# Kernel tuning notes

Hardware: AMD Instinct MI355X
Metric: run time of the kernel (lower is better)

## Reference

```python
import jax, jax.numpy as jnp
import numpy as np

RADIUS = 0.2
NPOINT = 1024
NSAMPLE = 32


def _square_distance(src, dst):
    # src [B,S,C], dst [B,N,C] -> [B,S,N]
    d = -2.0 * jnp.einsum('bsc,bnc->bsn', src, dst)
    d = d + jnp.sum(src * src, -1)[:, :, None]
    d = d + jnp.sum(dst * dst, -1)[:, None, :]
    return d


def _index_points(points, idx):
    # points [B,N,C], idx [B,...] int -> [B,...,C]
    B = points.shape[0]
    flat = idx.reshape(B, -1)
    out = jnp.take_along_axis(points, flat[:, :, None], axis=1)
    return out.reshape(idx.shape + (points.shape[-1],))


def _query_ball_point(radius, nsample, xyz, new_xyz):
    # xyz [B,N,C], new_xyz [B,S,C] -> idx [B,S,nsample]
    B, N, _ = xyz.shape
    sqd = _square_distance(new_xyz, xyz)            # [B,S,N]
    base = jnp.arange(N, dtype=jnp.int32)[None, None, :]
    idx = jnp.where(sqd > radius * radius, N, base)  # out-of-ball -> sentinel N
    idx = jnp.sort(idx, axis=-1)[:, :, :nsample]     # nearest-index nsample in ball
    first = idx[:, :, :1]
    idx = jnp.where(idx == N, first, idx)            # pad with first valid index
    return idx


def setup_inputs() -> dict:
    key = jax.random.key(0)
    ks = jax.random.split(key, 4)
    B, N, D = 8, 8192, 64
    xyz = jax.random.normal(ks[0], (B, 2, N), dtype=jnp.float32)
    points = jax.random.normal(ks[1], (B, D, N), dtype=jnp.float32)
    C_in = D + 2
    W1 = jax.random.normal(ks[2], (128, C_in), dtype=jnp.float32) * (1.0 / np.sqrt(C_in))
    b1 = jnp.zeros((128,), dtype=jnp.float32)
    W2 = jax.random.normal(ks[3], (256, 128), dtype=jnp.float32) * (1.0 / np.sqrt(128))
    b2 = jnp.zeros((256,), dtype=jnp.float32)
    return {"xyz": xyz, "points": points, "W1": W1, "b1": b1, "W2": W2, "b2": b2}


def reference(xyz, points, W1, b1, W2, b2):
    # xyz [B,2,N], points [B,D,N]
    xyz_t = jnp.transpose(xyz, (0, 2, 1))        # [B,N,2]
    pts_t = jnp.transpose(points, (0, 2, 1))     # [B,N,D]
    B, N, C = xyz_t.shape
    S = NPOINT
    # fps_idx = arange(npoint) in the source (deterministic sampling)
    new_xyz = xyz_t[:, :S, :]                    # [B,S,2]
    idx = _query_ball_point(RADIUS, NSAMPLE, xyz_t, new_xyz)   # [B,S,K]
    grouped_xyz = _index_points(xyz_t, idx)                    # [B,S,K,2]
    grouped_xyz_norm = grouped_xyz - new_xyz[:, :, None, :]
    grouped_pts = _index_points(pts_t, idx)                    # [B,S,K,D]
    feat = jnp.concatenate([grouped_xyz_norm, grouped_pts], axis=-1)  # [B,S,K,2+D]
    # permute(0,3,2,1) -> [B, C, K, S]; conv kernel (1,1) == pointwise linear on C
    h = jnp.transpose(feat, (0, 3, 2, 1))                      # [B,C,K,S]
    h = jax.nn.silu(jnp.einsum('bcks,oc->boks', h, W1) + b1[None, :, None, None])
    h = jax.nn.silu(jnp.einsum('bcks,oc->boks', h, W2) + b2[None, :, None, None])
    return h.mean(axis=2)                                      # [B, 256, S]
```

## Files before the change

### kernel.cpp

```cpp
#include <hip/hip_runtime.h>
#include <math.h>

#define BB 8
#define NN 8192
#define SS 1024
#define NS 32
#define DD 64
#define C1 128
#define C2 256
#define R2 0.04f
#define CPB 4

using bf16x8 = __attribute__((ext_vector_type(8))) short;
using f32x4  = __attribute__((ext_vector_type(4))) float;

__device__ __forceinline__ float rcp_f(float v) {
    float r; asm("v_rcp_f32 %0, %1" : "=v"(r) : "v"(v)); return r;
}
__device__ __forceinline__ float exp2_f(float v) {
    float r; asm("v_exp_f32 %0, %1" : "=v"(r) : "v"(v)); return r;
}
__device__ __forceinline__ float silu_f(float x) {
    return x * rcp_f(1.0f + exp2_f(x * -1.44269504088896f));
}
__device__ __forceinline__ unsigned int f2bf(float f) {
    unsigned int u = __float_as_uint(f);
    u += 0x7fffu + ((u >> 16) & 1u);
    return u >> 16;
}
__device__ __forceinline__ float bfl(unsigned int u) { return __uint_as_float(u << 16); }
__device__ __forceinline__ float bfh(unsigned int u) { return __uint_as_float(u & 0xffff0000u); }

__global__ __launch_bounds__(256) void qbp_kernel(const float* __restrict__ xyz,
                                                  int* __restrict__ idx_ws) {
    int gwave = (blockIdx.x * blockDim.x + threadIdx.x) >> 6;
    int lane  = threadIdx.x & 63;
    int b = gwave >> 10;
    int s = gwave & (SS - 1);
    const float* x = xyz + (size_t)b * 2 * NN;
    const float* y = x + NN;
    float cx = x[s], cy = y[s];
    float cs = __fadd_rn(__fmul_rn(cx, cx), __fmul_rn(cy, cy));
    int* ob = idx_ws + ((size_t)(b * SS + s)) * NS;

    float pxA = x[lane],      pyA = y[lane];
    float pxB = x[64 + lane], pyB = y[64 + lane];

    int written = 0;
    int first = -1;
    for (int base = 0; base < NN && written < NS; base += 128) {
        int jA2 = base + 128 + lane;      if (jA2 >= NN) jA2 = NN - 1;
        int jB2 = base + 192 + lane;      if (jB2 >= NN) jB2 = NN - 1;
        float nxA = x[jA2], nyA = y[jA2];
        float nxB = x[jB2], nyB = y[jB2];

        float ppA = __fadd_rn(__fmul_rn(pxA, pxA), __fmul_rn(pyA, pyA));
        float eA  = __fadd_rn(__fmul_rn(cx, pxA), __fmul_rn(cy, pyA));
        float dA  = __fadd_rn(__fadd_rn(__fmul_rn(-2.0f, eA), cs), ppA);
        float ppB = __fadd_rn(__fmul_rn(pxB, pxB), __fmul_rn(pyB, pyB));
        float eB  = __fadd_rn(__fmul_rn(cx, pxB), __fmul_rn(cy, pyB));
        float dB  = __fadd_rn(__fadd_rn(__fmul_rn(-2.0f, eB), cs), ppB);
        bool inA = !(dA > R2);
        bool inB = !(dB > R2);
        unsigned long long mA = __ballot(inA);
        unsigned long long mB = __ballot(inB);
        if (first < 0) {
            if (mA)      first = base + (__ffsll(mA) - 1);
            else if (mB) first = base + 64 + (__ffsll(mB) - 1);
        }
        unsigned long long below = (1ull << lane) - 1ull;
        int posA = __popcll(mA & below);
        if (inA && written + posA < NS) ob[written + posA] = base + lane;
        int wA = written + __popcll(mA);
        int posB = __popcll(mB & below);
        if (inB && wA + posB < NS) ob[wA + posB] = base + 64 + lane;
        written = wA + __popcll(mB);
        if (written > NS) written = NS;

        pxA = nxA; pyA = nyA; pxB = nxB; pyB = nyB;
    }
    if (lane >= written && lane < NS) ob[lane] = first;
}

__global__ __launch_bounds__(256) void pack_kernel(const float* __restrict__ W1,
                                                   const float* __restrict__ W2,
                                                   unsigned short* __restrict__ W1p,
                                                   unsigned short* __restrict__ W2p) {
    int bid = blockIdx.x;
    if (bid < 16) {
        int tid = bid * 256 + threadIdx.x;
        int l = tid & 63, frag = tid >> 6;
        int kb = frag >> 4, nt = frag & 15;
        int o  = nt * 16 + (l & 15);
        int c0 = kb * 32 + ((l >> 4) << 3);
        const float* src = W2 + (size_t)o * C1 + c0;
        unsigned int up[4];
        #pragma unroll
        for (int q = 0; q < 4; ++q)
            up[q] = f2bf(src[2 * q]) | (f2bf(src[2 * q + 1]) << 16);
        *(uint4*)(W2p + ((size_t)tid << 3)) = make_uint4(up[0], up[1], up[2], up[3]);
    } else {
        int tid = (bid - 16) * 256 + threadIdx.x;
        int l = tid & 63, frag = tid >> 6;
        int kb = frag >> 3, nt = frag & 7;
        int o  = nt * 16 + (l & 15);
        int c0 = kb * 32 + ((l >> 4) << 3);
        const float* src = W1 + (size_t)o * 66 + 2 + c0;
        unsigned int up[4];
        #pragma unroll
        for (int q = 0; q < 4; ++q)
            up[q] = f2bf(src[2 * q]) | (f2bf(src[2 * q + 1]) << 16);
        *(uint4*)(W1p + ((size_t)tid << 3)) = make_uint4(up[0], up[1], up[2], up[3]);
    }
}

__global__ __launch_bounds__(256) void p1g_kernel(const float* __restrict__ points,
                                                  const unsigned short* __restrict__ W1p,
                                                  const float* __restrict__ b1,
                                                  unsigned short* __restrict__ P1) {
    __shared__ __align__(16) char lds[34816];
    const int t = threadIdx.x;
    const int w = t >> 6, l = t & 63;
    const int bidx = blockIdx.x;
    const int b  = bidx >> 6;
    const int j0 = (bidx & 63) << 7;

    bf16x8 bfr[8][2];
    #pragma unroll
    for (int nt = 0; nt < 8; ++nt)
        #pragma unroll
        for (int kb = 0; kb < 2; ++kb)
            bfr[nt][kb] = *(const bf16x8*)(W1p + (((size_t)((kb * 8 + nt) * 64 + l)) << 3));
    float b1v[8];
    #pragma unroll
    for (int nt = 0; nt < 8; ++nt) b1v[nt] = b1[nt * 16 + (l & 15)];

    {
        const float* pb = points + (size_t)b * DD * NN + j0;
        int jj0 = (t & 31) * 4;
        #pragma unroll
        for (int i = 0; i < 4; ++i) {
            int c = 2 * ((t >> 5) + i * 8);
            float4 q0 = *(const float4*)(pb + (size_t)c * NN + jj0);
            float4 q1 = *(const float4*)(pb + (size_t)(c + 1) * NN + jj0);
            float a0[4] = {q0.x, q0.y, q0.z, q0.w};
            float a1[4] = {q1.x, q1.y, q1.z, q1.w};
            #pragma unroll
            for (int d = 0; d < 4; ++d) {
                int jj = jj0 + d;
                unsigned int u = f2bf(a0[d]) | (f2bf(a1[d]) << 16);
                unsigned int addr = ((unsigned)(jj * 128 + c * 2))
                                    ^ ((unsigned)((((jj & 7) ^ ((jj >> 2) & 7)) << 4)));
                *(unsigned int*)(lds + addr) = u;
            }
        }
    }
    __syncthreads();

    bf16x8 afr[2][2];
    #pragma unroll
    for (int mt = 0; mt < 2; ++mt)
        #pragma unroll
        for (int kb = 0; kb < 2; ++kb) {
            int jg = w * 32 + mt * 16 + (l & 15);
            unsigned int addr = ((unsigned)(jg * 128 + kb * 64 + ((l >> 4) << 4)))
                                ^ ((unsigned)((((jg & 7) ^ ((jg >> 2) & 7)) << 4)));
            afr[mt][kb] = *(const bf16x8*)(lds + addr);
        }
    __syncthreads();

    f32x4 acc[2][8];
    #pragma unroll
    for (int mt = 0; mt < 2; ++mt)
        #pragma unroll
        for (int nt = 0; nt < 8; ++nt) {
            f32x4 z4 = {0.0f, 0.0f, 0.0f, 0.0f};
            acc[mt][nt] = z4;
        }
    #pragma unroll
    for (int kb = 0; kb < 2; ++kb)
        #pragma unroll
        for (int mt = 0; mt < 2; ++mt)
            #pragma unroll
            for (int nt = 0; nt < 8; ++nt)
                acc[mt][nt] = __builtin_amdgcn_mfma_f32_16x16x32_bf16(
                    afr[mt][kb], bfr[nt][kb], acc[mt][nt], 0, 0, 0);

    #pragma unroll
    for (int mt = 0; mt < 2; ++mt)
        #pragma unroll
        for (int nt = 0; nt < 8; ++nt) {
            int row0 = w * 32 + mt * 16 + ((l >> 4) << 2);
            int col  = nt * 16 + (l & 15);
            #pragma unroll
            for (int r = 0; r < 4; ++r) {
                float v = acc[mt][nt][r] + b1v[nt];
                *(unsigned short*)(lds + (size_t)(row0 + r) * 272 + col * 2) =
                    (unsigned short)f2bf(v);
            }
        }
    __syncthreads();

    {
        int row = t >> 1, half = t & 1;
        const char* src = lds + (size_t)row * 272 + half * 128;
        unsigned short* dst = P1 + ((size_t)(b * NN + j0 + row)) * C1 + half * 64;
        #pragma unroll
        for (int i = 0; i < 8; ++i)
            *(uint4*)(dst + i * 8) = *(const uint4*)(src + i * 16);
    }
}

__global__ __launch_bounds__(256) void fused2_kernel(const float* __restrict__ xyz,
                                                     const float* __restrict__ W1,
                                                     const float* __restrict__ b2,
                                                     const unsigned short* __restrict__ P1,
                                                     const int* __restrict__ idx_ws,
                                                     const unsigned short* __restrict__ W2p,
                                                     float* __restrict__ tmp) {
    __shared__ __align__(16) unsigned short H1s[2][NS * C1];
    __shared__ int   idxs[CPB][NS];
    __shared__ float dxs[CPB][NS], dys[CPB][NS];
    __shared__ float w1xy[C1][2];

    const int t = threadIdx.x;
    const int w = t >> 6, l = t & 63;
    const int gc0 = blockIdx.x * CPB;
    const int b   = gc0 >> 10;

    if (t < C1) {
        w1xy[t][0] = W1[(size_t)t * 66 + 0];
        w1xy[t][1] = W1[(size_t)t * 66 + 1];
    }
    if (t < CPB * NS) {
        int ci = t >> 5, kk = t & 31;
        int gc = gc0 + ci;
        int s = gc & (SS - 1);
        const float* x = xyz + (size_t)b * 2 * NN;
        const float* y = x + NN;
        int j = idx_ws[(size_t)gc * NS + kk];
        idxs[ci][kk] = j;
        dxs[ci][kk] = x[j] - x[s];
        dys[ci][kk] = y[j] - y[s];
    }

    bf16x8 bfr[4][4];
    #pragma unroll
    for (int kb = 0; kb < 4; ++kb)
        #pragma unroll
        for (int ntl = 0; ntl < 4; ++ntl) {
            int nt = w * 4 + ntl;
            bfr[ntl][kb] = *(const bf16x8*)(W2p + ((size_t)((kb * 16 + nt) * 64 + l) << 3));
        }
    float b2v[4];
    #pragma unroll
    for (int ntl = 0; ntl < 4; ++ntl) b2v[ntl] = b2[w * 64 + ntl * 16 + (l & 15)];

    __syncthreads();

    const int k = t >> 3, cb = t & 7;
    float wx[16], wy[16];
    #pragma unroll
    for (int i = 0; i < 16; ++i) {
        wx[i] = w1xy[cb * 16 + i][0];
        wy[i] = w1xy[cb * 16 + i][1];
    }
    const unsigned int swz = (unsigned)((k & 7) << 4);
    const unsigned int sa0 = ((unsigned)(k * 256 + cb * 32)) ^ swz;
    const unsigned int sa1 = ((unsigned)(k * 256 + cb * 32 + 16)) ^ swz;
    unsigned int afr_addr[2][4];
    #pragma unroll
    for (int mt = 0; mt < 2; ++mt)
        #pragma unroll
        for (int kb = 0; kb < 4; ++kb) {
            int m = mt * 16 + (l & 15);
            afr_addr[mt][kb] = ((unsigned)(m * 256 + kb * 64 + ((l >> 4) << 4)))
                               ^ ((unsigned)((m & 7) << 4));
        }
    const unsigned short* P1b = P1 + (size_t)b * NN * C1 + cb * 16;

    for (int ci = -1; ci < CPB; ++ci) {
        const bool have = (ci + 1 < CPB);

        uint4 q0, q1; float dx = 0.0f, dy = 0.0f;
        if (have) {
            int j = idxs[ci + 1][k];
            dx = dxs[ci + 1][k]; dy = dys[ci + 1][k];
            const uint4* pr = (const uint4*)(P1b + (size_t)j * C1);
            q0 = pr[0]; q1 = pr[1];
        }

        if (ci >= 0) {
            const char* bufr = (const char*)H1s[ci & 1];
            bf16x8 afr[2][4];
            #pragma unroll
            for (int mt = 0; mt < 2; ++mt)
                #pragma unroll
                for (int kb = 0; kb < 4; ++kb)
                    afr[mt][kb] = *(const bf16x8*)(bufr + afr_addr[mt][kb]);
            f32x4 acc[2][4];
            #pragma unroll
            for (int mt = 0; mt < 2; ++mt)
                #pragma unroll
                for (int ntl = 0; ntl < 4; ++ntl) {
                    f32x4 z4 = {0.0f, 0.0f, 0.0f, 0.0f};
                    acc[mt][ntl] = z4;
                }
            #pragma unroll
            for (int kb = 0; kb < 4; ++kb)
                #pragma unroll
                for (int mt = 0; mt < 2; ++mt)
                    #pragma unroll
                    for (int ntl = 0; ntl < 4; ++ntl)
                        acc[mt][ntl] = __builtin_amdgcn_mfma_f32_16x16x32_bf16(
                            afr[mt][kb], bfr[ntl][kb], acc[mt][ntl], 0, 0, 0);
            float po[4];
            #pragma unroll
            for (int ntl = 0; ntl < 4; ++ntl) {
                float sum = 0.0f;
                #pragma unroll
                for (int mt = 0; mt < 2; ++mt)
                    #pragma unroll
                    for (int r = 0; r < 4; ++r)
                        sum += silu_f(acc[mt][ntl][r] + b2v[ntl]);
                sum += __shfl_xor(sum, 16);
                sum += __shfl_xor(sum, 32);
                po[ntl] = sum * (1.0f / 32.0f);
            }
            if (l < 16) {
                int gc = gc0 + ci;
                #pragma unroll
                for (int ntl = 0; ntl < 4; ++ntl)
                    tmp[(size_t)gc * C2 + w * 64 + ntl * 16 + l] = po[ntl];
            }
        }

        if (have) {
            float hv[16];
            hv[0]  = bfl(q0.x); hv[1]  = bfh(q0.x);
            hv[2]  = bfl(q0.y); hv[3]  = bfh(q0.y);
            hv[4]  = bfl(q0.z); hv[5]  = bfh(q0.z);
            hv[6]  = bfl(q0.w); hv[7]  = bfh(q0.w);
            hv[8]  = bfl(q1.x); hv[9]  = bfh(q1.x);
            hv[10] = bfl(q1.y); hv[11] = bfh(q1.y);
            hv[12] = bfl(q1.z); hv[13] = bfh(q1.z);
            hv[14] = bfl(q1.w); hv[15] = bfh(q1.w);
            #pragma unroll
            for (int i = 0; i < 16; ++i) {
                float v = hv[i] + wx[i] * dx + wy[i] * dy;
                hv[i] = silu_f(v);
            }
            unsigned int up[8];
            #pragma unroll
            for (int q = 0; q < 8; ++q)
                up[q] = f2bf(hv[2 * q]) | (f2bf(hv[2 * q + 1]) << 16);
            char* bufw = (char*)H1s[(ci + 1) & 1];
            *(uint4*)(bufw + sa0) = make_uint4(up[0], up[1], up[2], up[3]);
            *(uint4*)(bufw + sa1) = make_uint4(up[4], up[5], up[6], up[7]);
        }
        __syncthreads();
    }
}

__global__ __launch_bounds__(256) void transpose_kernel(const float* __restrict__ tmp,
                                                        float* __restrict__ out) {
    __shared__ float tile[32][33];
    int bid = blockIdx.x;
    int b  = bid >> 8;
    int r  = bid & 255;
    int s0 = (r >> 3) << 5;
    int o0 = (r & 7) << 5;
    int t = threadIdx.x;
    int c = t & 31, rr = t >> 5;
    const float* tb = tmp + (size_t)b * SS * C2;
    #pragma unroll
    for (int i = 0; i < 4; ++i) {
        int row = rr + i * 8;
        tile[row][c] = tb[(size_t)(s0 + row) * C2 + o0 + c];
    }
    __syncthreads();
    float* ob = out + (size_t)b * C2 * SS;
    #pragma unroll
    for (int i = 0; i < 4; ++i) {
        int row = rr + i * 8;
        ob[(size_t)(o0 + row) * SS + s0 + c] = tile[c][row];
    }
}

extern "C" void kernel_launch(void* const* d_in, const int* in_sizes, int n_in,
                              void* d_out, int out_size, void* d_ws, size_t ws_size,
                              hipStream_t stream) {
    const float* xyz    = (const float*)d_in[0];
    const float* points = (const float*)d_in[1];
    const float* W1     = (const float*)d_in[2];
    const float* b1     = (const float*)d_in[3];
    const float* W2     = (const float*)d_in[4];
    const float* b2     = (const float*)d_in[5];
    float* out = (float*)d_out;

    const size_t OFF_W1P = 65536;
    const size_t OFF_IDX = OFF_W1P + 16384;
    const size_t OFF_P1  = OFF_IDX + (size_t)BB * SS * NS * sizeof(int);
    const size_t OFF_TMP = OFF_P1 + (size_t)BB * NN * C1 * sizeof(unsigned short);

    unsigned short* W2p = (unsigned short*)d_ws;
    unsigned short* W1p = (unsigned short*)((char*)d_ws + OFF_W1P);
    int*            idx = (int*)((char*)d_ws + OFF_IDX);
    unsigned short* P1  = (unsigned short*)((char*)d_ws + OFF_P1);
    float*          tmp = (float*)((char*)d_ws + OFF_TMP);

    qbp_kernel   <<<BB * SS / 4,     256, 0, stream>>>(xyz, idx);
    pack_kernel  <<<20,              256, 0, stream>>>(W1, W2, W1p, W2p);
    p1g_kernel   <<<BB * (NN / 128), 256, 0, stream>>>(points, W1p, b1, P1);
    fused2_kernel<<<BB * SS / CPB,   256, 0, stream>>>(xyz, W1, b2, P1, idx, W2p, tmp);
    transpose_kernel<<<BB * (SS / 32) * (C2 / 32), 256, 0, stream>>>(tmp, out);
}
```

Measured before the change: 162.6 us.

## Fold weight packing into consumer kernels and stream A fragments per k-block

Removes the separate pack_kernel launch. The p1g and fused2 kernels now load fp32 W1/W2 directly and convert them to bf16 MFMA fragments in registers at kernel start. This saves one launch and its serial dependency, but every block repeats the strided fp32 loads and conversions. The W2 MFMA loop also loads the A fragments from LDS per k-block with unroll 1 instead of preloading all eight, which cuts register pressure at the cost of less latency hiding.

```diff
diff --git a/kernel.cpp b/kernel.cpp
--- a/kernel.cpp
+++ b/kernel.cpp
@@ -30,6 +30,14 @@
 }
 __device__ __forceinline__ float bfl(unsigned int u) { return __uint_as_float(u << 16); }
 __device__ __forceinline__ float bfh(unsigned int u) { return __uint_as_float(u & 0xffff0000u); }
+
+__device__ __forceinline__ bf16x8 frag8(const float* __restrict__ src) {
+    uint4 u = make_uint4(f2bf(src[0]) | (f2bf(src[1]) << 16),
+                         f2bf(src[2]) | (f2bf(src[3]) << 16),
+                         f2bf(src[4]) | (f2bf(src[5]) << 16),
+                         f2bf(src[6]) | (f2bf(src[7]) << 16));
+    return *(bf16x8*)&u;
+}
 
 __global__ __launch_bounds__(256) void qbp_kernel(const float* __restrict__ xyz,
                                                   int* __restrict__ idx_ws) {
@@ -82,40 +90,8 @@
     if (lane >= written && lane < NS) ob[lane] = first;
 }
 
-__global__ __launch_bounds__(256) void pack_kernel(const float* __restrict__ W1,
-                                                   const float* __restrict__ W2,
-                                                   unsigned short* __restrict__ W1p,
-                                                   unsigned short* __restrict__ W2p) {
-    int bid = blockIdx.x;
-    if (bid < 16) {
-        int tid = bid * 256 + threadIdx.x;
-        int l = tid & 63, frag = tid >> 6;
-        int kb = frag >> 4, nt = frag & 15;
-        int o  = nt * 16 + (l & 15);
-        int c0 = kb * 32 + ((l >> 4) << 3);
-        const float* src = W2 + (size_t)o * C1 + c0;
-        unsigned int up[4];
-        #pragma unroll
-        for (int q = 0; q < 4; ++q)
-            up[q] = f2bf(src[2 * q]) | (f2bf(src[2 * q + 1]) << 16);
-        *(uint4*)(W2p + ((size_t)tid << 3)) = make_uint4(up[0], up[1], up[2], up[3]);
-    } else {
-        int tid = (bid - 16) * 256 + threadIdx.x;
-        int l = tid & 63, frag = tid >> 6;
-        int kb = frag >> 3, nt = frag & 7;
-        int o  = nt * 16 + (l & 15);
-        int c0 = kb * 32 + ((l >> 4) << 3);
-        const float* src = W1 + (size_t)o * 66 + 2 + c0;
-        unsigned int up[4];
-        #pragma unroll
-        for (int q = 0; q < 4; ++q)
-            up[q] = f2bf(src[2 * q]) | (f2bf(src[2 * q + 1]) << 16);
-        *(uint4*)(W1p + ((size_t)tid << 3)) = make_uint4(up[0], up[1], up[2], up[3]);
-    }
-}
-
 __global__ __launch_bounds__(256) void p1g_kernel(const float* __restrict__ points,
-                                                  const unsigned short* __restrict__ W1p,
+                                                  const float* __restrict__ W1,
                                                   const float* __restrict__ b1,
                                                   unsigned short* __restrict__ P1) {
     __shared__ __align__(16) char lds[34816];
@@ -129,8 +105,11 @@
     #pragma unroll
     for (int nt = 0; nt < 8; ++nt)
         #pragma unroll
-        for (int kb = 0; kb < 2; ++kb)
-            bfr[nt][kb] = *(const bf16x8*)(W1p + (((size_t)((kb * 8 + nt) * 64 + l)) << 3));
+        for (int kb = 0; kb < 2; ++kb) {
+            int o  = nt * 16 + (l & 15);
+            int c0 = kb * 32 + ((l >> 4) << 3);
+            bfr[nt][kb] = frag8(W1 + (size_t)o * 66 + 2 + c0);
+        }
     float b1v[8];
     #pragma unroll
     for (int nt = 0; nt < 8; ++nt) b1v[nt] = b1[nt * 16 + (l & 15)];
@@ -213,10 +192,10 @@
 
 __global__ __launch_bounds__(256) void fused2_kernel(const float* __restrict__ xyz,
                                                      const float* __restrict__ W1,
+                                                     const float* __restrict__ W2,
                                                      const float* __restrict__ b2,
                                                      const unsigned short* __restrict__ P1,
                                                      const int* __restrict__ idx_ws,
-                                                     const unsigned short* __restrict__ W2p,
                                                      float* __restrict__ tmp) {
     __shared__ __align__(16) unsigned short H1s[2][NS * C1];
     __shared__ int   idxs[CPB][NS];
@@ -249,8 +228,9 @@
     for (int kb = 0; kb < 4; ++kb)
         #pragma unroll
         for (int ntl = 0; ntl < 4; ++ntl) {
-            int nt = w * 4 + ntl;
-            bfr[ntl][kb] = *(const bf16x8*)(W2p + ((size_t)((kb * 16 + nt) * 64 + l) << 3));
+            int o  = (w * 4 + ntl) * 16 + (l & 15);
+            int c0 = kb * 32 + ((l >> 4) << 3);
+            bfr[ntl][kb] = frag8(W2 + (size_t)o * C1 + c0);
         }
     float b2v[4];
     #pragma unroll
@@ -292,12 +272,6 @@
 
         if (ci >= 0) {
             const char* bufr = (const char*)H1s[ci & 1];
-            bf16x8 afr[2][4];
-            #pragma unroll
-            for (int mt = 0; mt < 2; ++mt)
-                #pragma unroll
-                for (int kb = 0; kb < 4; ++kb)
-                    afr[mt][kb] = *(const bf16x8*)(bufr + afr_addr[mt][kb]);
             f32x4 acc[2][4];
             #pragma unroll
             for (int mt = 0; mt < 2; ++mt)
@@ -306,14 +280,18 @@
                     f32x4 z4 = {0.0f, 0.0f, 0.0f, 0.0f};
                     acc[mt][ntl] = z4;
                 }
-            #pragma unroll
-            for (int kb = 0; kb < 4; ++kb)
+            #pragma unroll 1
+            for (int kb = 0; kb < 4; ++kb) {
+                bf16x8 a0 = *(const bf16x8*)(bufr + afr_addr[0][kb]);
+                bf16x8 a1 = *(const bf16x8*)(bufr + afr_addr[1][kb]);
                 #pragma unroll
-                for (int mt = 0; mt < 2; ++mt)
-                    #pragma unroll
-                    for (int ntl = 0; ntl < 4; ++ntl)
-                        acc[mt][ntl] = __builtin_amdgcn_mfma_f32_16x16x32_bf16(
-                            afr[mt][kb], bfr[ntl][kb], acc[mt][ntl], 0, 0, 0);
+                for (int ntl = 0; ntl < 4; ++ntl) {
+                    acc[0][ntl] = __builtin_amdgcn_mfma_f32_16x16x32_bf16(
+                        a0, bfr[ntl][kb], acc[0][ntl], 0, 0, 0);
+                    acc[1][ntl] = __builtin_amdgcn_mfma_f32_16x16x32_bf16(
+                        a1, bfr[ntl][kb], acc[1][ntl], 0, 0, 0);
+                }
+            }
             float po[4];
             #pragma unroll
             for (int ntl = 0; ntl < 4; ++ntl) {
@@ -398,20 +376,15 @@
     const float* b2     = (const float*)d_in[5];
     float* out = (float*)d_out;
 
-    const size_t OFF_W1P = 65536;
-    const size_t OFF_IDX = OFF_W1P + 16384;
-    const size_t OFF_P1  = OFF_IDX + (size_t)BB * SS * NS * sizeof(int);
+    const size_t OFF_P1  = (size_t)BB * SS * NS * sizeof(int);
     const size_t OFF_TMP = OFF_P1 + (size_t)BB * NN * C1 * sizeof(unsigned short);
 
-    unsigned short* W2p = (unsigned short*)d_ws;
-    unsigned short* W1p = (unsigned short*)((char*)d_ws + OFF_W1P);
-    int*            idx = (int*)((char*)d_ws + OFF_IDX);
+    int*            idx = (int*)d_ws;
     unsigned short* P1  = (unsigned short*)((char*)d_ws + OFF_P1);
     float*          tmp = (float*)((char*)d_ws + OFF_TMP);
 
     qbp_kernel   <<<BB * SS / 4,     256, 0, stream>>>(xyz, idx);
-    pack_kernel  <<<20,              256, 0, stream>>>(W1, W2, W1p, W2p);
-    p1g_kernel   <<<BB * (NN / 128), 256, 0, stream>>>(points, W1p, b1, P1);
-    fused2_kernel<<<BB * SS / CPB,   256, 0, stream>>>(xyz, W1, b2, P1, idx, W2p, tmp);
+    p1g_kernel   <<<BB * (NN / 128), 256, 0, stream>>>(points, W1, b1, P1);
+    fused2_kernel<<<BB * SS / CPB,   256, 0, stream>>>(xyz, W1, W2, b2, P1, idx, tmp);
     transpose_kernel<<<BB * (SS / 32) * (C2 / 32), 256, 0, stream>>>(tmp, out);
 }
```

Measured after the change: 239.4 us. 47.3% more time.
